# Optimization experiments

Hardware: AMD Instinct MI355X
Metric: run time of the kernel (lower is better)

## Reference

```python
import jax, jax.numpy as jnp
import numpy as np

D_MODEL = 1024
NUM_HEADS = 16
D_K = D_MODEL // NUM_HEADS
NEG_INF = -1.0e9


def setup_inputs() -> dict:
    key = jax.random.key(0)
    ks = jax.random.split(key, 12)
    B, S = 2, 2048
    s = 1.0 / np.sqrt(D_MODEL)
    return {
        "q": jax.random.normal(ks[0], (B, S, D_MODEL), jnp.float32),
        "k": jax.random.normal(ks[1], (B, S, D_MODEL), jnp.float32),
        "v": jax.random.normal(ks[2], (B, S, D_MODEL), jnp.float32),
        "encoder_mask": jnp.ones((B, 1, 1, S), jnp.int32),
        "W_q": jax.random.normal(ks[3], (D_MODEL, D_MODEL), jnp.float32) * s,
        "b_q": jnp.zeros((D_MODEL,), jnp.float32),
        "W_k": jax.random.normal(ks[4], (D_MODEL, D_MODEL), jnp.float32) * s,
        "b_k": jnp.zeros((D_MODEL,), jnp.float32),
        "W_v": jax.random.normal(ks[5], (D_MODEL, D_MODEL), jnp.float32) * s,
        "b_v": jnp.zeros((D_MODEL,), jnp.float32),
        "W_o": jax.random.normal(ks[6], (D_MODEL, D_MODEL), jnp.float32) * s,
        "b_o": jnp.zeros((D_MODEL,), jnp.float32),
    }


def reference(q, k, v, encoder_mask, W_q, b_q, W_k, b_k, W_v, b_v, W_o, b_o):
    B, S, _ = q.shape
    # projections (torch Linear: x @ W^T + b)
    def proj(x, W, b):
        y = x @ W.T + b
        return y.reshape(B, -1, NUM_HEADS, D_K).transpose(0, 2, 1, 3)  # [B,H,S,dk]

    Q = proj(q, W_q, b_q)
    K = proj(k, W_k, b_k)
    V = proj(v, W_v, b_v)

    scores = jnp.einsum("bhqd,bhkd->bhqk", Q, K) / jnp.sqrt(jnp.float32(D_K))
    scores = jnp.where(encoder_mask == 0, NEG_INF, scores)
    # NOTE: source module computes softmax(scores) but then (bug) multiplies
    # the raw masked scores by V; softmax result is dead code, so we skip it.
    attn_out = jnp.einsum("bhqk,bhkd->bhqd", scores, V)
    attn_out = attn_out.transpose(0, 2, 1, 3).reshape(B, S, D_MODEL)
    return attn_out @ W_o.T + b_o
```

## Files before the change

kernel.cpp:

```cpp
#include <hip/hip_runtime.h>
#include <stdint.h>

#define DM 1024
#define NH 16
#define DK 64

typedef __attribute__((ext_vector_type(8))) __bf16 bf16x8;
typedef __attribute__((ext_vector_type(4))) float f32x4;

__device__ __forceinline__ float bf2f(unsigned short u) {
    union { uint32_t i; float f; } x; x.i = ((uint32_t)u) << 16; return x.f;
}
__device__ __forceinline__ unsigned short f2bf(float f) {
    union { float f; uint32_t i; } x; x.f = f;
    uint32_t r = x.i + 0x7fffu + ((x.i >> 16) & 1u);
    return (unsigned short)(r >> 16);
}

__device__ __forceinline__ void gl2lds16(const void* g, void* l) {
    __builtin_amdgcn_global_load_lds(
        (const __attribute__((address_space(1))) void*)g,
        (__attribute__((address_space(3))) void*)l, 16, 0, 0);
}

__device__ __forceinline__ f32x4 mfma_bf16(bf16x8 a, bf16x8 b, f32x4 c) {
    return __builtin_amdgcn_mfma_f32_16x16x32_bf16(a, b, c, 0, 0, 0);
}

__device__ __forceinline__ void store_out(float* p, float v) { *p = v; }
__device__ __forceinline__ void store_out(unsigned short* p, float v) { *p = f2bf(v); }

struct CvtArgs {
    const float* src[16];
    unsigned short* dst[16];
};

__global__ __launch_bounds__(256) void cvt16(CvtArgs a) {
    const int t = blockIdx.x * 256 + threadIdx.x;
    const int seg = t >> 18;
    const int off = t & 0x3ffff;
    const float4 v = reinterpret_cast<const float4*>(a.src[seg])[off];
    ushort4 o;
    o.x = f2bf(v.x); o.y = f2bf(v.y); o.z = f2bf(v.z); o.w = f2bf(v.w);
    reinterpret_cast<ushort4*>(a.dst[seg])[off] = o;
}

template<typename OutT>
struct GemmArgs {
    const unsigned short* A[3];
    const unsigned short* W[3];
    const float* bias[3];
    OutT* C[3];
};

template<int BM, int BN, typename OutT>
__global__ __launch_bounds__(256) void gemm_nt_bf16(GemmArgs<OutT> g, int M, int N, int K)
{
    const unsigned short* __restrict__ A  = g.A[blockIdx.z];
    const unsigned short* __restrict__ Bw = g.W[blockIdx.z];
    const float* __restrict__ bias = g.bias[blockIdx.z];
    OutT* __restrict__ C = g.C[blockIdx.z];

    constexpr int FM = BM / 32;
    constexpr int FN = BN / 32;

    __shared__ unsigned short As[BM * 64];
    __shared__ unsigned short Bs[BN * 64];

    const int tid  = threadIdx.x;
    const int lane = tid & 63;
    const int w    = tid >> 6;
    const int wr   = w >> 1, wc = w & 1;
    const int row0 = blockIdx.y * BM;
    const int col0 = blockIdx.x * BN;

    f32x4 acc[FM][FN];
    #pragma unroll
    for (int m = 0; m < FM; ++m)
        #pragma unroll
        for (int n = 0; n < FN; ++n)
            acc[m][n] = (f32x4){0.f, 0.f, 0.f, 0.f};

    const int srow = lane >> 3;
    const int scol = (lane & 7) * 8;

    for (int kt = 0; kt < K; kt += 64) {
        #pragma unroll
        for (int i = 0; i < BM / 32; ++i) {
            const int stripe = w * (BM / 32) + i;
            const int r = stripe * 8 + srow;
            gl2lds16(A + (size_t)(row0 + r) * K + kt + scol, &As[stripe * 512]);
        }
        #pragma unroll
        for (int i = 0; i < BN / 32; ++i) {
            const int stripe = w * (BN / 32) + i;
            const int r = stripe * 8 + srow;
            gl2lds16(Bw + (size_t)(col0 + r) * K + kt + scol, &Bs[stripe * 512]);
        }
        __syncthreads();

        #pragma unroll
        for (int kk = 0; kk < 2; ++kk) {
            const int ko = kk * 32 + (lane >> 4) * 8;
            bf16x8 af[FM], bf[FN];
            #pragma unroll
            for (int m = 0; m < FM; ++m)
                af[m] = *reinterpret_cast<const bf16x8*>(
                    &As[(wr * (BM / 2) + m * 16 + (lane & 15)) * 64 + ko]);
            #pragma unroll
            for (int n = 0; n < FN; ++n)
                bf[n] = *reinterpret_cast<const bf16x8*>(
                    &Bs[(wc * (BN / 2) + n * 16 + (lane & 15)) * 64 + ko]);
            #pragma unroll
            for (int m = 0; m < FM; ++m)
                #pragma unroll
                for (int n = 0; n < FN; ++n)
                    acc[m][n] = mfma_bf16(af[m], bf[n], acc[m][n]);
        }
        __syncthreads();
    }

    const int cr = (lane >> 4) * 4;
    const int cc = lane & 15;
    #pragma unroll
    for (int n = 0; n < FN; ++n) {
        const int col = col0 + wc * (BN / 2) + n * 16 + cc;
        const float bv = bias[col];
        #pragma unroll
        for (int m = 0; m < FM; ++m) {
            const int rowb = row0 + wr * (BM / 2) + m * 16 + cr;
            #pragma unroll
            for (int r = 0; r < 4; ++r)
                store_out(&C[(size_t)(rowb + r) * N + col], acc[m][n][r] + bv);
        }
    }
}

__global__ __launch_bounds__(256) void ktv_partial(
    const unsigned short* __restrict__ Kb, const unsigned short* __restrict__ Vb,
    const int* __restrict__ mask, float* __restrict__ Mpart,
    float* __restrict__ cvpart, int S, int schunk)
{
    __shared__ float Ks[16][64];
    __shared__ float Vs[16][64];
    __shared__ float cvs[16][64];
    const int bh = blockIdx.x, chunk = blockIdx.y, BH = gridDim.x;
    const int b = bh >> 4, h = bh & 15;
    const int tid = threadIdx.x;
    const int tx = tid & 15, ty = tid >> 4;
    const int s0 = chunk * schunk;

    float acc[4][4] = {};
    float cv[4] = {0.f, 0.f, 0.f, 0.f};

    for (int sc = 0; sc < schunk; sc += 16) {
        const int s = s0 + sc + ty;
        const size_t rowoff = (size_t)(b * S + s) * DM + h * DK + tx * 4;
        const ushort4 kraw = *reinterpret_cast<const ushort4*>(Kb + rowoff);
        const ushort4 vraw = *reinterpret_cast<const ushort4*>(Vb + rowoff);
        float kv[4] = {bf2f(kraw.x), bf2f(kraw.y), bf2f(kraw.z), bf2f(kraw.w)};
        const float vv[4] = {bf2f(vraw.x), bf2f(vraw.y), bf2f(vraw.z), bf2f(vraw.w)};
        if (mask[b * S + s] == 0) {
            #pragma unroll
            for (int j = 0; j < 4; ++j) { cv[j] += vv[j]; kv[j] = 0.f; }
        }
        __syncthreads();
        #pragma unroll
        for (int j = 0; j < 4; ++j) { Ks[ty][tx * 4 + j] = kv[j]; Vs[ty][tx * 4 + j] = vv[j]; }
        __syncthreads();
        #pragma unroll
        for (int ss = 0; ss < 16; ++ss) {
            float kvv[4], vvv[4];
            #pragma unroll
            for (int i = 0; i < 4; ++i) kvv[i] = Ks[ss][ty * 4 + i];
            #pragma unroll
            for (int j = 0; j < 4; ++j) vvv[j] = Vs[ss][tx * 4 + j];
            #pragma unroll
            for (int i = 0; i < 4; ++i)
                #pragma unroll
                for (int j = 0; j < 4; ++j)
                    acc[i][j] += kvv[i] * vvv[j];
        }
    }

    const size_t mbase = ((size_t)chunk * BH + bh) * (DK * DK);
    #pragma unroll
    for (int i = 0; i < 4; ++i)
        #pragma unroll
        for (int j = 0; j < 4; ++j)
            Mpart[mbase + (size_t)(ty * 4 + i) * DK + tx * 4 + j] = acc[i][j];

    __syncthreads();
    #pragma unroll
    for (int j = 0; j < 4; ++j) cvs[ty][tx * 4 + j] = cv[j];
    __syncthreads();
    if (tid < DK) {
        float s = 0.f;
        #pragma unroll
        for (int r = 0; r < 16; ++r) s += cvs[r][tid];
        cvpart[((size_t)chunk * BH + bh) * DK + tid] = s;
    }
}

__global__ __launch_bounds__(256) void reduce_m(
    const float* __restrict__ Mpart, const float* __restrict__ cvpart,
    float* __restrict__ Mm, float* __restrict__ cvec, int nchunk, int BH)
{
    const int bh = blockIdx.x;
    const int tid = threadIdx.x;
    const int e0 = blockIdx.y * 512;
    for (int e = e0 + tid; e < e0 + 512; e += 256) {
        float s = 0.f;
        for (int c = 0; c < nchunk; ++c)
            s += Mpart[((size_t)c * BH + bh) * (DK * DK) + e];
        Mm[(size_t)bh * DK * DK + e] = s * 0.125f;
    }
    if (blockIdx.y == 0 && tid < DK) {
        float s = 0.f;
        for (int c = 0; c < nchunk; ++c)
            s += cvpart[((size_t)c * BH + bh) * DK + tid];
        cvec[bh * DK + tid] = s;
    }
}

__global__ __launch_bounds__(256) void qm_attn(
    const unsigned short* __restrict__ Qb, const float* __restrict__ Mm,
    const float* __restrict__ cvec, unsigned short* __restrict__ attn, int S)
{
    __shared__ float Qs[64][65];
    __shared__ float Ms[64][65];
    const int bh = blockIdx.y;
    const int b = bh >> 4, h = bh & 15;
    const int s0 = blockIdx.x * 64;
    const int tid = threadIdx.x;
    const int tx = tid & 15, ty = tid >> 4;
    const int lr = tid >> 2;
    const int lc = tid & 3;

    #pragma unroll
    for (int u = 0; u < 4; ++u) {
        const int f = (lc + u * 4) * 4;
        const ushort4 qraw = *reinterpret_cast<const ushort4*>(
            Qb + (size_t)(b * S + s0 + lr) * DM + h * DK + f);
        Qs[lr][f + 0] = bf2f(qraw.x); Qs[lr][f + 1] = bf2f(qraw.y);
        Qs[lr][f + 2] = bf2f(qraw.z); Qs[lr][f + 3] = bf2f(qraw.w);
        const float4 mv = *reinterpret_cast<const float4*>(
            Mm + (size_t)bh * DK * DK + (size_t)lr * DK + f);
        Ms[lr][f + 0] = mv.x; Ms[lr][f + 1] = mv.y; Ms[lr][f + 2] = mv.z; Ms[lr][f + 3] = mv.w;
    }
    __syncthreads();

    float acc[4][4] = {};
    #pragma unroll 8
    for (int kk = 0; kk < 64; ++kk) {
        float qv[4], mv[4];
        #pragma unroll
        for (int i = 0; i < 4; ++i) qv[i] = Qs[ty * 4 + i][kk];
        #pragma unroll
        for (int j = 0; j < 4; ++j) mv[j] = Ms[kk][tx * 4 + j];
        #pragma unroll
        for (int i = 0; i < 4; ++i)
            #pragma unroll
            for (int j = 0; j < 4; ++j)
                acc[i][j] += qv[i] * mv[j];
    }

    float cvv[4];
    #pragma unroll
    for (int j = 0; j < 4; ++j) cvv[j] = -1.0e9f * cvec[bh * DK + tx * 4 + j];

    #pragma unroll
    for (int i = 0; i < 4; ++i) {
        const size_t orow = (size_t)(b * S + s0 + ty * 4 + i) * DM + h * DK;
        ushort4 o;
        o.x = f2bf(acc[i][0] + cvv[0]);
        o.y = f2bf(acc[i][1] + cvv[1]);
        o.z = f2bf(acc[i][2] + cvv[2]);
        o.w = f2bf(acc[i][3] + cvv[3]);
        *reinterpret_cast<ushort4*>(&attn[orow + tx * 4]) = o;
    }
}

extern "C" void kernel_launch(void* const* d_in, const int* in_sizes, int n_in,
                              void* d_out, int out_size, void* d_ws, size_t ws_size,
                              hipStream_t stream)
{
    const float* q    = (const float*)d_in[0];
    const float* k    = (const float*)d_in[1];
    const float* v    = (const float*)d_in[2];
    const int*   mask = (const int*)  d_in[3];
    const float* Wq   = (const float*)d_in[4];
    const float* bq   = (const float*)d_in[5];
    const float* Wk   = (const float*)d_in[6];
    const float* bk   = (const float*)d_in[7];
    const float* Wv   = (const float*)d_in[8];
    const float* bv   = (const float*)d_in[9];
    const float* Wo   = (const float*)d_in[10];
    const float* bo   = (const float*)d_in[11];
    float* out = (float*)d_out;

    const int BS = in_sizes[0] / DM;
    const int B  = 2;
    const int S  = BS / B;
    const int BH = B * NH;
    const int SCHUNK = 64;
    const int NCHUNK = S / SCHUNK;
    const size_t BSDM = (size_t)BS * DM;
    const size_t DMDM = (size_t)DM * DM;

    unsigned short* ws = (unsigned short*)d_ws;
    unsigned short* qb   = ws;
    unsigned short* kb   = qb  + BSDM;
    unsigned short* vb   = kb  + BSDM;
    unsigned short* Wqb  = vb  + BSDM;
    unsigned short* Wkb  = Wqb + DMDM;
    unsigned short* Wvb  = Wkb + DMDM;
    unsigned short* Wob  = Wvb + DMDM;
    unsigned short* Qp   = Wob + DMDM;
    unsigned short* Kp   = Qp  + BSDM;
    unsigned short* Vp   = Kp  + BSDM;
    unsigned short* attnb = qb;
    float* Mpart = (float*)kb;
    float* cvprt = (float*)Wqb;
    float* Mm    = cvprt + (size_t)NCHUNK * BH * DK;
    float* cvec  = Mm    + (size_t)BH * DK * DK;

    const dim3 blk(256);

    CvtArgs cv;
    for (int i = 0; i < 4; ++i) { cv.src[0+i] = q + (size_t)i * DMDM; cv.dst[0+i] = qb + (size_t)i * DMDM; }
    for (int i = 0; i < 4; ++i) { cv.src[4+i] = k + (size_t)i * DMDM; cv.dst[4+i] = kb + (size_t)i * DMDM; }
    for (int i = 0; i < 4; ++i) { cv.src[8+i] = v + (size_t)i * DMDM; cv.dst[8+i] = vb + (size_t)i * DMDM; }
    cv.src[12] = Wq; cv.dst[12] = Wqb;
    cv.src[13] = Wk; cv.dst[13] = Wkb;
    cv.src[14] = Wv; cv.dst[14] = Wvb;
    cv.src[15] = Wo; cv.dst[15] = Wob;
    cvt16<<<dim3(16 * 1024), blk, 0, stream>>>(cv);

    GemmArgs<unsigned short> ga;
    ga.A[0] = qb;  ga.A[1] = kb;  ga.A[2] = vb;
    ga.W[0] = Wqb; ga.W[1] = Wkb; ga.W[2] = Wvb;
    ga.bias[0] = bq; ga.bias[1] = bk; ga.bias[2] = bv;
    ga.C[0] = Qp;  ga.C[1] = Kp;  ga.C[2] = Vp;
    gemm_nt_bf16<128, 128, unsigned short>
        <<<dim3(DM / 128, BS / 128, 3), blk, 0, stream>>>(ga, BS, DM, DM);

    ktv_partial<<<dim3(BH, NCHUNK), blk, 0, stream>>>(Kp, Vp, mask, Mpart, cvprt, S, SCHUNK);
    reduce_m<<<dim3(BH, 8), blk, 0, stream>>>(Mpart, cvprt, Mm, cvec, NCHUNK, BH);

    qm_attn<<<dim3(S / 64, BH), blk, 0, stream>>>(Qp, Mm, cvec, attnb, S);

    GemmArgs<float> gf;
    gf.A[0] = attnb; gf.A[1] = nullptr; gf.A[2] = nullptr;
    gf.W[0] = Wob;   gf.W[1] = nullptr; gf.W[2] = nullptr;
    gf.bias[0] = bo; gf.bias[1] = nullptr; gf.bias[2] = nullptr;
    gf.C[0] = out;   gf.C[1] = nullptr;  gf.C[2] = nullptr;
    gemm_nt_bf16<128, 64, float>
        <<<dim3(DM / 64, BS / 128, 1), blk, 0, stream>>>(gf, BS, DM, DM);
}
```

Before: 145.0 us.

## Fold per-head KV matrix into output projection and pipeline QKV GEMM

Replaces the QKV projection GEMM with a 256x256-tile, 512-thread kernel that double-buffers global-to-LDS loads in half-tile steps, using explicit waitcnt, barriers and priority hints. The per-head K^T V matrix and the mask-bias vector are folded algebraically into a per-batch fused output weight and bias. The final GEMM can then consume Q directly, which removes the qm_attn kernel and the separate conversion of Wo. The fused weight is rounded to bf16, which adds extra rounding error, and the bias fold runs as a scalar dot-product kernel.

```diff
diff --git a/kernel.cpp b/kernel.cpp
--- a/kernel.cpp
+++ b/kernel.cpp
@@ -27,15 +27,19 @@
     return __builtin_amdgcn_mfma_f32_16x16x32_bf16(a, b, c, 0, 0, 0);
 }
 
-__device__ __forceinline__ void store_out(float* p, float v) { *p = v; }
-__device__ __forceinline__ void store_out(unsigned short* p, float v) { *p = f2bf(v); }
+template<int N> __device__ __forceinline__ void waitvm() {
+    if constexpr (N == 8)      asm volatile("s_waitcnt vmcnt(8)" ::: "memory");
+    else if constexpr (N == 4) asm volatile("s_waitcnt vmcnt(4)" ::: "memory");
+    else if constexpr (N == 0) asm volatile("s_waitcnt vmcnt(0)" ::: "memory");
+    else                       asm volatile("" ::: "memory");
+}
 
 struct CvtArgs {
-    const float* src[16];
-    unsigned short* dst[16];
+    const float* src[15];
+    unsigned short* dst[15];
 };
 
-__global__ __launch_bounds__(256) void cvt16(CvtArgs a) {
+__global__ __launch_bounds__(256) void cvt15(CvtArgs a) {
     const int t = blockIdx.x * 256 + threadIdx.x;
     const int seg = t >> 18;
     const int off = t & 0x3ffff;
@@ -45,22 +49,184 @@
     reinterpret_cast<ushort4*>(a.dst[seg])[off] = o;
 }
 
-template<typename OutT>
-struct GemmArgs {
+struct Gemm8Args {
     const unsigned short* A[3];
     const unsigned short* W[3];
     const float* bias[3];
-    OutT* C[3];
+    unsigned short* C[3];
 };
 
-template<int BM, int BN, typename OutT>
-__global__ __launch_bounds__(256) void gemm_nt_bf16(GemmArgs<OutT> g, int M, int N, int K)
+__device__ __forceinline__ void stage_half2(const unsigned short* src, int ldg,
+                                            unsigned short* dst, int tid) {
+    gl2lds16(src,                        dst + (size_t)tid * 8);
+    gl2lds16(src + (size_t)ldg * 128,    dst + 4096 + (size_t)tid * 8);
+}
+
+template<bool I1, bool I2, bool I3, bool I4, int W2, int W4>
+__device__ __forceinline__ void tile_step(
+    int t, int K, const unsigned short* aSrc, const unsigned short* bSrc,
+    unsigned short* ldsBase, int tid, int aOff, int bOff,
+    bf16x8 (&af)[8], f32x4 (&acc)[8][4])
+{
+    const int par = t & 1;
+    unsigned short* L  = ldsBase + par * 32768;
+    unsigned short* Ln = ldsBase + (par ^ 1) * 32768;
+    const unsigned short* A0 = L;
+    const unsigned short* A1 = L + 8192;
+    const unsigned short* B0 = L + 16384;
+    const unsigned short* B1 = L + 24576;
+
+    {
+        #pragma unroll
+        for (int m = 0; m < 8; ++m)
+            af[m] = *reinterpret_cast<const bf16x8*>(A0 + m * 512 + aOff);
+        bf16x8 b0 = *reinterpret_cast<const bf16x8*>(B0 + 0 * 512 + bOff);
+        bf16x8 b1 = *reinterpret_cast<const bf16x8*>(B0 + 1 * 512 + bOff);
+        if (I1) stage_half2(aSrc + (size_t)(t + 1) * 64 + 32, K, Ln + 8192, tid);
+        __builtin_amdgcn_s_barrier();
+        asm volatile("s_waitcnt lgkmcnt(0)" ::: "memory");
+        __builtin_amdgcn_sched_barrier(0);
+        __builtin_amdgcn_s_setprio(1);
+        #pragma unroll
+        for (int m = 0; m < 8; ++m) {
+            acc[m][0] = mfma_bf16(af[m], b0, acc[m][0]);
+            acc[m][1] = mfma_bf16(af[m], b1, acc[m][1]);
+        }
+        __builtin_amdgcn_s_setprio(0);
+        waitvm<-1>();
+        __builtin_amdgcn_s_barrier();
+        __builtin_amdgcn_sched_barrier(0);
+    }
+    {
+        bf16x8 b0 = *reinterpret_cast<const bf16x8*>(B0 + 2 * 512 + bOff);
+        bf16x8 b1 = *reinterpret_cast<const bf16x8*>(B0 + 3 * 512 + bOff);
+        if (I2) stage_half2(bSrc + (size_t)(t + 1) * 64 + 32, K, Ln + 24576, tid);
+        __builtin_amdgcn_s_barrier();
+        asm volatile("s_waitcnt lgkmcnt(0)" ::: "memory");
+        __builtin_amdgcn_sched_barrier(0);
+        __builtin_amdgcn_s_setprio(1);
+        #pragma unroll
+        for (int m = 0; m < 8; ++m) {
+            acc[m][2] = mfma_bf16(af[m], b0, acc[m][2]);
+            acc[m][3] = mfma_bf16(af[m], b1, acc[m][3]);
+        }
+        __builtin_amdgcn_s_setprio(0);
+        waitvm<W2>();
+        __builtin_amdgcn_s_barrier();
+        __builtin_amdgcn_sched_barrier(0);
+    }
+    {
+        #pragma unroll
+        for (int m = 0; m < 8; ++m)
+            af[m] = *reinterpret_cast<const bf16x8*>(A1 + m * 512 + aOff);
+        bf16x8 b0 = *reinterpret_cast<const bf16x8*>(B1 + 0 * 512 + bOff);
+        bf16x8 b1 = *reinterpret_cast<const bf16x8*>(B1 + 1 * 512 + bOff);
+        if (I3) stage_half2(aSrc + (size_t)(t + 2) * 64, K, L, tid);
+        __builtin_amdgcn_s_barrier();
+        asm volatile("s_waitcnt lgkmcnt(0)" ::: "memory");
+        __builtin_amdgcn_sched_barrier(0);
+        __builtin_amdgcn_s_setprio(1);
+        #pragma unroll
+        for (int m = 0; m < 8; ++m) {
+            acc[m][0] = mfma_bf16(af[m], b0, acc[m][0]);
+            acc[m][1] = mfma_bf16(af[m], b1, acc[m][1]);
+        }
+        __builtin_amdgcn_s_setprio(0);
+        waitvm<-1>();
+        __builtin_amdgcn_s_barrier();
+        __builtin_amdgcn_sched_barrier(0);
+    }
+    {
+        bf16x8 b0 = *reinterpret_cast<const bf16x8*>(B1 + 2 * 512 + bOff);
+        bf16x8 b1 = *reinterpret_cast<const bf16x8*>(B1 + 3 * 512 + bOff);
+        if (I4) stage_half2(bSrc + (size_t)(t + 2) * 64, K, L + 16384, tid);
+        __builtin_amdgcn_s_barrier();
+        asm volatile("s_waitcnt lgkmcnt(0)" ::: "memory");
+        __builtin_amdgcn_sched_barrier(0);
+        __builtin_amdgcn_s_setprio(1);
+        #pragma unroll
+        for (int m = 0; m < 8; ++m) {
+            acc[m][2] = mfma_bf16(af[m], b0, acc[m][2]);
+            acc[m][3] = mfma_bf16(af[m], b1, acc[m][3]);
+        }
+        __builtin_amdgcn_s_setprio(0);
+        waitvm<W4>();
+        __builtin_amdgcn_s_barrier();
+        __builtin_amdgcn_sched_barrier(0);
+    }
+}
+
+__global__ __launch_bounds__(512, 2) void gemm8_nt_bf16(Gemm8Args g, int M, int N, int K)
 {
     const unsigned short* __restrict__ A  = g.A[blockIdx.z];
     const unsigned short* __restrict__ Bw = g.W[blockIdx.z];
     const float* __restrict__ bias = g.bias[blockIdx.z];
-    OutT* __restrict__ C = g.C[blockIdx.z];
-
+    unsigned short* __restrict__ C = g.C[blockIdx.z];
+
+    __shared__ unsigned short lds[2][4][8192];
+
+    const int tid  = threadIdx.x;
+    const int lane = tid & 63;
+    const int w    = tid >> 6;
+    const int wr   = w >> 2, wc = w & 3;
+    const int l15  = lane & 15, q8 = (lane >> 4) * 8;
+    const int row0 = blockIdx.y * 256;
+    const int col0 = blockIdx.x * 256;
+
+    const unsigned short* aSrc = A  + (size_t)(row0 + (tid >> 2)) * K + (tid & 3) * 8;
+    const unsigned short* bSrc = Bw + (size_t)(col0 + (tid >> 2)) * K + (tid & 3) * 8;
+    unsigned short* ldsBase = &lds[0][0][0];
+
+    const int aOff = (wr * 128 + l15) * 32 + q8;
+    const int bOff = (wc * 64  + l15) * 32 + q8;
+
+    f32x4 acc[8][4];
+    #pragma unroll
+    for (int m = 0; m < 8; ++m)
+        #pragma unroll
+        for (int n = 0; n < 4; ++n)
+            acc[m][n] = (f32x4){0.f, 0.f, 0.f, 0.f};
+    bf16x8 af[8];
+
+    const int NT = K >> 6;
+
+    stage_half2(aSrc,      K, ldsBase,             tid);
+    stage_half2(bSrc,      K, ldsBase + 16384,     tid);
+    stage_half2(aSrc + 32, K, ldsBase + 8192,      tid);
+    stage_half2(bSrc + 32, K, ldsBase + 24576,     tid);
+    stage_half2(aSrc + 64, K, ldsBase + 32768,     tid);
+    stage_half2(bSrc + 64, K, ldsBase + 32768 + 16384, tid);
+    waitvm<8>();
+    __builtin_amdgcn_s_barrier();
+    __builtin_amdgcn_sched_barrier(0);
+
+    for (int t = 0; t < NT - 2; ++t)
+        tile_step<true, true, true, true, 8, 8>(t, K, aSrc, bSrc, ldsBase, tid, aOff, bOff, af, acc);
+    tile_step<true, true, false, false, 8, 4>(NT - 2, K, aSrc, bSrc, ldsBase, tid, aOff, bOff, af, acc);
+    tile_step<false, false, false, false, 0, -1>(NT - 1, K, aSrc, bSrc, ldsBase, tid, aOff, bOff, af, acc);
+
+    const int cr = (lane >> 4) * 4, cc = lane & 15;
+    #pragma unroll
+    for (int n = 0; n < 4; ++n) {
+        const int col = col0 + wc * 64 + n * 16 + cc;
+        const float bv = bias[col];
+        #pragma unroll
+        for (int m = 0; m < 8; ++m) {
+            const int rowb = row0 + wr * 128 + m * 16 + cr;
+            #pragma unroll
+            for (int r = 0; r < 4; ++r)
+                C[(size_t)(rowb + r) * N + col] = f2bf(acc[m][n][r] + bv);
+        }
+    }
+}
+
+template<int BM, int BN>
+__global__ __launch_bounds__(256) void gemm_nt_final(
+    const unsigned short* __restrict__ A,
+    const unsigned short* __restrict__ W0, const unsigned short* __restrict__ W1,
+    const float* __restrict__ bias0, const float* __restrict__ bias1,
+    float* __restrict__ C, int M, int N, int K, int rowSplit)
+{
     constexpr int FM = BM / 32;
     constexpr int FN = BN / 32;
 
@@ -73,6 +239,9 @@
     const int wr   = w >> 1, wc = w & 1;
     const int row0 = blockIdx.y * BM;
     const int col0 = blockIdx.x * BN;
+    const bool hi  = row0 >= rowSplit;
+    const unsigned short* __restrict__ Bw = hi ? W1 : W0;
+    const float* __restrict__ bias = hi ? bias1 : bias0;
 
     f32x4 acc[FM][FN];
     #pragma unroll
@@ -102,20 +271,20 @@
         #pragma unroll
         for (int kk = 0; kk < 2; ++kk) {
             const int ko = kk * 32 + (lane >> 4) * 8;
-            bf16x8 af[FM], bf[FN];
+            bf16x8 afr[FM], bfr[FN];
             #pragma unroll
             for (int m = 0; m < FM; ++m)
-                af[m] = *reinterpret_cast<const bf16x8*>(
+                afr[m] = *reinterpret_cast<const bf16x8*>(
                     &As[(wr * (BM / 2) + m * 16 + (lane & 15)) * 64 + ko]);
             #pragma unroll
             for (int n = 0; n < FN; ++n)
-                bf[n] = *reinterpret_cast<const bf16x8*>(
+                bfr[n] = *reinterpret_cast<const bf16x8*>(
                     &Bs[(wc * (BN / 2) + n * 16 + (lane & 15)) * 64 + ko]);
             #pragma unroll
             for (int m = 0; m < FM; ++m)
                 #pragma unroll
                 for (int n = 0; n < FN; ++n)
-                    acc[m][n] = mfma_bf16(af[m], bf[n], acc[m][n]);
+                    acc[m][n] = mfma_bf16(afr[m], bfr[n], acc[m][n]);
         }
         __syncthreads();
     }
@@ -131,7 +300,7 @@
             const int rowb = row0 + wr * (BM / 2) + m * 16 + cr;
             #pragma unroll
             for (int r = 0; r < 4; ++r)
-                store_out(&C[(size_t)(rowb + r) * N + col], acc[m][n][r] + bv);
+                C[(size_t)(rowb + r) * N + col] = acc[m][n][r] + bv;
         }
     }
 }
@@ -223,62 +392,83 @@
     }
 }
 
-__global__ __launch_bounds__(256) void qm_attn(
-    const unsigned short* __restrict__ Qb, const float* __restrict__ Mm,
-    const float* __restrict__ cvec, unsigned short* __restrict__ attn, int S)
-{
-    __shared__ float Qs[64][65];
-    __shared__ float Ms[64][65];
-    const int bh = blockIdx.y;
-    const int b = bh >> 4, h = bh & 15;
-    const int s0 = blockIdx.x * 64;
-    const int tid = threadIdx.x;
-    const int tx = tid & 15, ty = tid >> 4;
-    const int lr = tid >> 2;
-    const int lc = tid & 3;
-
-    #pragma unroll
-    for (int u = 0; u < 4; ++u) {
-        const int f = (lc + u * 4) * 4;
-        const ushort4 qraw = *reinterpret_cast<const ushort4*>(
-            Qb + (size_t)(b * S + s0 + lr) * DM + h * DK + f);
-        Qs[lr][f + 0] = bf2f(qraw.x); Qs[lr][f + 1] = bf2f(qraw.y);
-        Qs[lr][f + 2] = bf2f(qraw.z); Qs[lr][f + 3] = bf2f(qraw.w);
-        const float4 mv = *reinterpret_cast<const float4*>(
-            Mm + (size_t)bh * DK * DK + (size_t)lr * DK + f);
-        Ms[lr][f + 0] = mv.x; Ms[lr][f + 1] = mv.y; Ms[lr][f + 2] = mv.z; Ms[lr][f + 3] = mv.w;
-    }
-    __syncthreads();
-
-    float acc[4][4] = {};
-    #pragma unroll 8
-    for (int kk = 0; kk < 64; ++kk) {
-        float qv[4], mv[4];
-        #pragma unroll
-        for (int i = 0; i < 4; ++i) qv[i] = Qs[ty * 4 + i][kk];
-        #pragma unroll
-        for (int j = 0; j < 4; ++j) mv[j] = Ms[kk][tx * 4 + j];
-        #pragma unroll
-        for (int i = 0; i < 4; ++i)
-            #pragma unroll
-            for (int j = 0; j < 4; ++j)
-                acc[i][j] += qv[i] * mv[j];
-    }
-
-    float cvv[4];
-    #pragma unroll
-    for (int j = 0; j < 4; ++j) cvv[j] = -1.0e9f * cvec[bh * DK + tx * 4 + j];
-
-    #pragma unroll
-    for (int i = 0; i < 4; ++i) {
-        const size_t orow = (size_t)(b * S + s0 + ty * 4 + i) * DM + h * DK;
-        ushort4 o;
-        o.x = f2bf(acc[i][0] + cvv[0]);
-        o.y = f2bf(acc[i][1] + cvv[1]);
-        o.z = f2bf(acc[i][2] + cvv[2]);
-        o.w = f2bf(acc[i][3] + cvv[3]);
-        *reinterpret_cast<ushort4*>(&attn[orow + tx * 4]) = o;
-    }
+__device__ __forceinline__ bf16x8 ld_cvt8(const float* p) {
+    const float4 x = *reinterpret_cast<const float4*>(p);
+    const float4 y = *reinterpret_cast<const float4*>(p + 4);
+    union { unsigned short u[8]; bf16x8 v; } r;
+    r.u[0] = f2bf(x.x); r.u[1] = f2bf(x.y); r.u[2] = f2bf(x.z); r.u[3] = f2bf(x.w);
+    r.u[4] = f2bf(y.x); r.u[5] = f2bf(y.y); r.u[6] = f2bf(y.z); r.u[7] = f2bf(y.w);
+    return r.v;
+}
+
+__global__ __launch_bounds__(256) void fuse_w(
+    const float* __restrict__ Mm, const float* __restrict__ Wo,
+    unsigned short* __restrict__ Wf)
+{
+    const int h = blockIdx.y;
+    const int b = blockIdx.z;
+    const int o0 = blockIdx.x * 256;
+    const int tid = threadIdx.x, lane = tid & 63, w = tid >> 6;
+    const int l15 = lane & 15, q8 = (lane >> 4) * 8;
+    const float* MmH = Mm + (size_t)(b * NH + h) * (DK * DK);
+
+    f32x4 acc[4][4];
+    #pragma unroll
+    for (int m = 0; m < 4; ++m)
+        #pragma unroll
+        for (int n = 0; n < 4; ++n)
+            acc[m][n] = (f32x4){0.f, 0.f, 0.f, 0.f};
+
+    bf16x8 af[4][2], bf[4][2];
+    #pragma unroll
+    for (int m = 0; m < 4; ++m) {
+        const int orow = o0 + w * 64 + m * 16 + l15;
+        #pragma unroll
+        for (int kk = 0; kk < 2; ++kk)
+            af[m][kk] = ld_cvt8(Wo + (size_t)orow * DM + h * DK + kk * 32 + q8);
+    }
+    #pragma unroll
+    for (int n = 0; n < 4; ++n) {
+        const int d = n * 16 + l15;
+        #pragma unroll
+        for (int kk = 0; kk < 2; ++kk)
+            bf[n][kk] = ld_cvt8(MmH + (size_t)d * DK + kk * 32 + q8);
+    }
+    #pragma unroll
+    for (int kk = 0; kk < 2; ++kk)
+        #pragma unroll
+        for (int m = 0; m < 4; ++m)
+            #pragma unroll
+            for (int n = 0; n < 4; ++n)
+                acc[m][n] = mfma_bf16(af[m][kk], bf[n][kk], acc[m][n]);
+
+    const int cr = (lane >> 4) * 4, cc = lane & 15;
+    #pragma unroll
+    for (int n = 0; n < 4; ++n)
+        #pragma unroll
+        for (int m = 0; m < 4; ++m)
+            #pragma unroll
+            for (int r = 0; r < 4; ++r)
+                Wf[(size_t)b * DM * DM +
+                   (size_t)(o0 + w * 64 + m * 16 + cr + r) * DM +
+                   h * DK + n * 16 + cc] = f2bf(acc[m][n][r]);
+}
+
+__global__ __launch_bounds__(256) void fuse_bias(
+    const float* __restrict__ cvec, const float* __restrict__ Wo,
+    const float* __restrict__ bo, float* __restrict__ bias2)
+{
+    const int t = blockIdx.x * 256 + threadIdx.x;
+    const int b = t >> 10, o = t & 1023;
+    const float* cv = cvec + (b << 10);
+    const float* wr = Wo + (size_t)o * DM;
+    float s = 0.f;
+    for (int j = 0; j < DM; j += 4) {
+        const float4 c4 = *reinterpret_cast<const float4*>(cv + j);
+        const float4 w4 = *reinterpret_cast<const float4*>(wr + j);
+        s += c4.x * w4.x + c4.y * w4.y + c4.z * w4.z + c4.w * w4.w;
+    }
+    bias2[t] = bo[o] - 1.0e9f * s;
 }
 
 extern "C" void kernel_launch(void* const* d_in, const int* in_sizes, int n_in,
@@ -315,46 +505,40 @@
     unsigned short* Wqb  = vb  + BSDM;
     unsigned short* Wkb  = Wqb + DMDM;
     unsigned short* Wvb  = Wkb + DMDM;
-    unsigned short* Wob  = Wvb + DMDM;
-    unsigned short* Qp   = Wob + DMDM;
+    unsigned short* Qp   = Wvb + DMDM;
     unsigned short* Kp   = Qp  + BSDM;
     unsigned short* Vp   = Kp  + BSDM;
-    unsigned short* attnb = qb;
     float* Mpart = (float*)kb;
     float* cvprt = (float*)Wqb;
     float* Mm    = cvprt + (size_t)NCHUNK * BH * DK;
     float* cvec  = Mm    + (size_t)BH * DK * DK;
+    unsigned short* Wf = qb;
+    float* bias2 = (float*)Wkb;
 
     const dim3 blk(256);
 
     CvtArgs cv;
-    for (int i = 0; i < 4; ++i) { cv.src[0+i] = q + (size_t)i * DMDM; cv.dst[0+i] = qb + (size_t)i * DMDM; }
-    for (int i = 0; i < 4; ++i) { cv.src[4+i] = k + (size_t)i * DMDM; cv.dst[4+i] = kb + (size_t)i * DMDM; }
-    for (int i = 0; i < 4; ++i) { cv.src[8+i] = v + (size_t)i * DMDM; cv.dst[8+i] = vb + (size_t)i * DMDM; }
+    for (int i = 0; i < 4; ++i) { cv.src[0 + i] = q + (size_t)i * DMDM; cv.dst[0 + i] = qb + (size_t)i * DMDM; }
+    for (int i = 0; i < 4; ++i) { cv.src[4 + i] = k + (size_t)i * DMDM; cv.dst[4 + i] = kb + (size_t)i * DMDM; }
+    for (int i = 0; i < 4; ++i) { cv.src[8 + i] = v + (size_t)i * DMDM; cv.dst[8 + i] = vb + (size_t)i * DMDM; }
     cv.src[12] = Wq; cv.dst[12] = Wqb;
     cv.src[13] = Wk; cv.dst[13] = Wkb;
     cv.src[14] = Wv; cv.dst[14] = Wvb;
-    cv.src[15] = Wo; cv.dst[15] = Wob;
-    cvt16<<<dim3(16 * 1024), blk, 0, stream>>>(cv);
-
-    GemmArgs<unsigned short> ga;
+    cvt15<<<dim3(15 * 1024), blk, 0, stream>>>(cv);
+
+    Gemm8Args ga;
     ga.A[0] = qb;  ga.A[1] = kb;  ga.A[2] = vb;
     ga.W[0] = Wqb; ga.W[1] = Wkb; ga.W[2] = Wvb;
     ga.bias[0] = bq; ga.bias[1] = bk; ga.bias[2] = bv;
     ga.C[0] = Qp;  ga.C[1] = Kp;  ga.C[2] = Vp;
-    gemm_nt_bf16<128, 128, unsigned short>
-        <<<dim3(DM / 128, BS / 128, 3), blk, 0, stream>>>(ga, BS, DM, DM);
+    gemm8_nt_bf16<<<dim3(DM / 256, BS / 256, 3), dim3(512), 0, stream>>>(ga, BS, DM, DM);
 
     ktv_partial<<<dim3(BH, NCHUNK), blk, 0, stream>>>(Kp, Vp, mask, Mpart, cvprt, S, SCHUNK);
     reduce_m<<<dim3(BH, 8), blk, 0, stream>>>(Mpart, cvprt, Mm, cvec, NCHUNK, BH);
 
-    qm_attn<<<dim3(S / 64, BH), blk, 0, stream>>>(Qp, Mm, cvec, attnb, S);
-
-    GemmArgs<float> gf;
-    gf.A[0] = attnb; gf.A[1] = nullptr; gf.A[2] = nullptr;
-    gf.W[0] = Wob;   gf.W[1] = nullptr; gf.W[2] = nullptr;
-    gf.bias[0] = bo; gf.bias[1] = nullptr; gf.bias[2] = nullptr;
-    gf.C[0] = out;   gf.C[1] = nullptr;  gf.C[2] = nullptr;
-    gemm_nt_bf16<128, 64, float>
-        <<<dim3(DM / 64, BS / 128, 1), blk, 0, stream>>>(gf, BS, DM, DM);
-}
+    fuse_w<<<dim3(DM / 256, NH, B), blk, 0, stream>>>(Mm, Wo, Wf);
+    fuse_bias<<<dim3(B * DM / 256), blk, 0, stream>>>(cvec, Wo, bo, bias2);
+
+    gemm_nt_final<128, 64><<<dim3(DM / 64, BS / 128), blk, 0, stream>>>(
+        Qp, Wf, Wf + DMDM, bias2, bias2 + DM, out, BS, DM, DM, S);
+}
```

Result: slower. 163.1 us (+12.5%).
